# Kernel optimization log

Measured on AMD Instinct MI355X. Metric: run time of the kernel, lower is better.

The kernel has to match this reference:

```python
import jax, jax.numpy as jnp
import numpy as np

STRIDE = 1
PADDING = 1
KERNEL = 3


def _extract_patches(x, k, stride, padding):
    # x: [N, C, H, W] -> patches stacked as [k, k, N, C, Hout, Wout]
    xp = jnp.pad(x, ((0, 0), (0, 0), (padding, padding), (padding, padding)))
    Hp, Wp = xp.shape[2], xp.shape[3]
    oh = (Hp - k) // stride + 1
    ow = (Wp - k) // stride + 1
    rows = []
    for i in range(k):
        cols = []
        for j in range(k):
            cols.append(xp[:, :, i : i + oh * stride : stride, j : j + ow * stride : stride])
        rows.append(jnp.stack(cols, axis=0))
    return jnp.stack(rows, axis=0)  # [k, k, N, C, oh, ow]


def setup_inputs() -> dict:
    key = jax.random.key(0)
    k1, k2 = jax.random.split(key)
    N, C, H, W = 32, 32, 56, 56
    O, OH, OW, K = 32, 56, 56, 3
    x = jax.random.normal(k1, (N, C, H, W), dtype=jnp.float32)
    # kaiming-normal-ish scale for leaky_relu(a=0.1), fan_out mode
    fan_out = O * K * K
    gain = np.sqrt(2.0 / (1.0 + 0.1 ** 2))
    std = gain / np.sqrt(fan_out)
    weight = jax.random.normal(k2, (O, OH, OW, C, K, K), dtype=jnp.float32) * std
    bias = jnp.zeros((1, O, OH, OW), dtype=jnp.float32)
    return {"x": x, "weight": weight, "bias": bias}


def reference(x, weight, bias):
    # weight: [O, H, W, C, i, k]; patches: [i, k, N, C, H, W]
    patches = _extract_patches(x, KERNEL, STRIDE, PADDING)
    out = jnp.einsum('ohwcik,iknchw->nohw', weight, patches)
    return out + bias
```

## Files before the change

kernel.cpp:

```cpp
#include <hip/hip_runtime.h>

#define N_  32
#define C_  32
#define H_  56
#define W_  56
#define O_  32
#define HP_ 58
#define WP_ 58
#define HW_ (H_*W_)
#define CHW_ (C_*H_*W_)
#define KK_ 9
#define CKK_ (C_*KK_)

#define XT_FLOATS ((size_t)C_*HP_*WP_*N_)

typedef __bf16 bf16x8 __attribute__((ext_vector_type(8)));
typedef float  f32x4  __attribute__((ext_vector_type(4)));

__global__ __launch_bounds__(256) void xpose_kernel(const float* __restrict__ x,
                                                    float* __restrict__ xT) {
    const int c = blockIdx.x;
    const int y = blockIdx.y;
    __shared__ float sbuf[32 * 57];
    const int tid = threadIdx.x;
    const bool interior = (y >= 1) && (y <= H_);
    if (interior) {
        for (int idx = tid; idx < N_ * W_; idx += 256) {
            int n = idx / W_;
            int col = idx - n * W_;
            sbuf[n * 57 + col] = x[((size_t)(n * C_ + c) * H_ + (y - 1)) * W_ + col];
        }
    }
    __syncthreads();
    float* dst = xT + ((size_t)(c * HP_ + y)) * WP_ * N_;
    for (int idx = tid; idx < WP_ * N_; idx += 256) {
        int xx = idx >> 5;
        int n  = idx & 31;
        float v = 0.f;
        if (interior && xx >= 1 && xx <= W_) v = sbuf[n * 57 + (xx - 1)];
        dst[idx] = v;
    }
}

__global__ __launch_bounds__(256) void lc2d_mfma(const float* __restrict__ wgt,
                                                 const float* __restrict__ xT,
                                                 const float* __restrict__ bias,
                                                 float* __restrict__ out) {
    __shared__ int offs[288];
    __shared__ __align__(16) float sbuf[32][33][4];

    const int tid = threadIdx.x;
    for (int k = tid; k < 288; k += 256) {
        int c = k / 9, ij = k - 9 * c;
        int i = ij / 3, j = ij - 3 * i;
        offs[k] = c * (HP_ * WP_ * N_) + i * (WP_ * N_) + j * N_;
    }
    __syncthreads();

    const int flat = blockIdx.x;
    const int wg = (flat & 7) * 98 + (flat >> 3);
    const int wt = wg % 14;
    const int h  = wg / 14;
    const int wave = tid >> 6;
    const int lane = tid & 63;
    const int w = wt * 4 + wave;
    const int q = lane >> 4;
    const int r = lane & 15;

    const float* wb0 = wgt + ((size_t)(r * HW_ + h * W_ + w)) * CKK_ + 8 * q;
    const float* wb1 = wb0 + (size_t)16 * HW_ * CKK_;
    const float* ab = xT + (h * WP_ + w) * N_ + r;

    f32x4 acc00 = {0.f,0.f,0.f,0.f}, acc01 = {0.f,0.f,0.f,0.f};
    f32x4 acc10 = {0.f,0.f,0.f,0.f}, acc11 = {0.f,0.f,0.f,0.f};

    #pragma unroll 3
    for (int s = 0; s < 9; ++s) {
        const int4 ov0 = *(const int4*)&offs[32 * s + 8 * q];
        const int4 ov1 = *(const int4*)&offs[32 * s + 8 * q + 4];
        const float4 b0a = *(const float4*)(wb0 + 32 * s);
        const float4 b0b = *(const float4*)(wb0 + 32 * s + 4);
        const float4 b1a = *(const float4*)(wb1 + 32 * s);
        const float4 b1b = *(const float4*)(wb1 + 32 * s + 4);

        const int offv[8] = {ov0.x, ov0.y, ov0.z, ov0.w, ov1.x, ov1.y, ov1.z, ov1.w};
        float a0[8], a1[8];
        #pragma unroll
        for (int t = 0; t < 8; ++t) {
            const float* p = ab + offv[t];
            a0[t] = p[0];
            a1[t] = p[16];
        }

        bf16x8 af0, af1, bf0, bf1;
        #pragma unroll
        for (int t = 0; t < 8; ++t) {
            af0[t] = (__bf16)a0[t];
            af1[t] = (__bf16)a1[t];
        }
        bf0[0] = (__bf16)b0a.x; bf0[1] = (__bf16)b0a.y; bf0[2] = (__bf16)b0a.z; bf0[3] = (__bf16)b0a.w;
        bf0[4] = (__bf16)b0b.x; bf0[5] = (__bf16)b0b.y; bf0[6] = (__bf16)b0b.z; bf0[7] = (__bf16)b0b.w;
        bf1[0] = (__bf16)b1a.x; bf1[1] = (__bf16)b1a.y; bf1[2] = (__bf16)b1a.z; bf1[3] = (__bf16)b1a.w;
        bf1[4] = (__bf16)b1b.x; bf1[5] = (__bf16)b1b.y; bf1[6] = (__bf16)b1b.z; bf1[7] = (__bf16)b1b.w;

        acc00 = __builtin_amdgcn_mfma_f32_16x16x32_bf16(af0, bf0, acc00, 0, 0, 0);
        acc01 = __builtin_amdgcn_mfma_f32_16x16x32_bf16(af0, bf1, acc01, 0, 0, 0);
        acc10 = __builtin_amdgcn_mfma_f32_16x16x32_bf16(af1, bf0, acc10, 0, 0, 0);
        acc11 = __builtin_amdgcn_mfma_f32_16x16x32_bf16(af1, bf1, acc11, 0, 0, 0);
    }

    #pragma unroll
    for (int mt = 0; mt < 2; ++mt) {
        #pragma unroll
        for (int ot = 0; ot < 2; ++ot) {
            f32x4 a = (mt == 0) ? (ot == 0 ? acc00 : acc01)
                                : (ot == 0 ? acc10 : acc11);
            const int o = ot * 16 + r;
            #pragma unroll
            for (int reg = 0; reg < 4; ++reg) {
                const int n = mt * 16 + q * 4 + reg;
                sbuf[n][o][wave] = a[reg];
            }
        }
    }
    __syncthreads();

    const int w0 = wt * 4;
    #pragma unroll
    for (int rr = 0; rr < 4; ++rr) {
        const int fl = rr * 256 + tid;
        const int n = fl >> 5;
        const int o = fl & 31;
        float4 v = *(const float4*)&sbuf[n][o][0];
        const float4 bv = *(const float4*)(bias + o * HW_ + h * W_ + w0);
        v.x += bv.x; v.y += bv.y; v.z += bv.z; v.w += bv.w;
        *(float4*)(out + (size_t)n * CHW_ + o * HW_ + h * W_ + w0) = v;
    }
}

__global__ __launch_bounds__(256) void lc2d_naive(const float* __restrict__ x,
                                                  const float* __restrict__ wgt,
                                                  const float* __restrict__ bias,
                                                  float* __restrict__ out) {
    int idx = blockIdx.x * 256 + threadIdx.x;
    const int total = N_ * O_ * H_ * W_;
    if (idx >= total) return;
    int w = idx % W_;
    int h = (idx / W_) % H_;
    int o = (idx / HW_) % O_;
    int n = idx / CHW_;
    const float* wp = wgt + ((size_t)((o * H_ + h) * W_ + w)) * CKK_;
    float s = 0.f;
    for (int c = 0; c < C_; ++c) {
        for (int i = 0; i < 3; ++i) {
            int yy = h + i - 1;
            if (yy < 0 || yy >= H_) continue;
            for (int j = 0; j < 3; ++j) {
                int xx = w + j - 1;
                if (xx < 0 || xx >= W_) continue;
                s = fmaf(wp[c * KK_ + i * 3 + j],
                         x[((size_t)(n * C_ + c) * H_ + yy) * W_ + xx], s);
            }
        }
    }
    out[idx] = s + bias[idx % CHW_];
}

extern "C" void kernel_launch(void* const* d_in, const int* in_sizes, int n_in,
                              void* d_out, int out_size, void* d_ws, size_t ws_size,
                              hipStream_t stream) {
    const float* x    = (const float*)d_in[0];
    const float* wgt  = (const float*)d_in[1];
    const float* bias = (const float*)d_in[2];
    float* out = (float*)d_out;

    const size_t need = XT_FLOATS * sizeof(float);
    if (ws_size >= need) {
        float* xT = (float*)d_ws;
        hipLaunchKernelGGL(xpose_kernel, dim3(C_, HP_), dim3(256), 0, stream, x, xT);
        hipLaunchKernelGGL(lc2d_mfma, dim3(784), dim3(256), 0, stream, wgt, xT, bias, out);
    } else {
        int total = N_ * O_ * H_ * W_;
        hipLaunchKernelGGL(lc2d_naive, dim3((total + 255) / 256), dim3(256), 0, stream,
                           x, wgt, bias, out);
    }
}
```

Measured before the change: 45.37 us.

## Store transposed input as bf16 and split output channels across waves

The transpose kernel now writes the padded input workspace in bf16 rather than fp32. This halves its write and gather traffic and removes the per-element conversions in the main kernel. The MFMA kernel is also repartitioned: each block covers 2 output columns instead of 4, and each wave handles one 16-channel half of the outputs with 2 MFMAs instead of 4. The grid doubles to 1568 blocks and the epilogue uses float2 stores. The weight stream is unchanged, and the narrower output stores may coalesce less well.

```diff
diff --git a/kernel.cpp b/kernel.cpp
--- a/kernel.cpp
+++ b/kernel.cpp
@@ -12,13 +12,13 @@
 #define KK_ 9
 #define CKK_ (C_*KK_)
 
-#define XT_FLOATS ((size_t)C_*HP_*WP_*N_)
+#define XT_ELEMS ((size_t)C_*HP_*WP_*N_)
 
 typedef __bf16 bf16x8 __attribute__((ext_vector_type(8)));
 typedef float  f32x4  __attribute__((ext_vector_type(4)));
 
 __global__ __launch_bounds__(256) void xpose_kernel(const float* __restrict__ x,
-                                                    float* __restrict__ xT) {
+                                                    __bf16* __restrict__ xT) {
     const int c = blockIdx.x;
     const int y = blockIdx.y;
     __shared__ float sbuf[32 * 57];
@@ -32,22 +32,22 @@
         }
     }
     __syncthreads();
-    float* dst = xT + ((size_t)(c * HP_ + y)) * WP_ * N_;
+    __bf16* dst = xT + ((size_t)(c * HP_ + y)) * WP_ * N_;
     for (int idx = tid; idx < WP_ * N_; idx += 256) {
         int xx = idx >> 5;
         int n  = idx & 31;
         float v = 0.f;
         if (interior && xx >= 1 && xx <= W_) v = sbuf[n * 57 + (xx - 1)];
-        dst[idx] = v;
+        dst[idx] = (__bf16)v;
     }
 }
 
 __global__ __launch_bounds__(256) void lc2d_mfma(const float* __restrict__ wgt,
-                                                 const float* __restrict__ xT,
+                                                 const __bf16* __restrict__ xT,
                                                  const float* __restrict__ bias,
                                                  float* __restrict__ out) {
     __shared__ int offs[288];
-    __shared__ __align__(16) float sbuf[32][33][4];
+    __shared__ __align__(16) float sbuf[32][33][2];
 
     const int tid = threadIdx.x;
     for (int k = tid; k < 288; k += 256) {
@@ -58,83 +58,67 @@
     __syncthreads();
 
     const int flat = blockIdx.x;
-    const int wg = (flat & 7) * 98 + (flat >> 3);
-    const int wt = wg % 14;
-    const int h  = wg / 14;
+    const int wg = (flat & 7) * 196 + (flat >> 3);
+    const int wt = wg % 28;
+    const int h  = wg / 28;
     const int wave = tid >> 6;
     const int lane = tid & 63;
-    const int w = wt * 4 + wave;
+    const int dw = wave & 1;
+    const int oh = wave >> 1;
+    const int w  = wt * 2 + dw;
     const int q = lane >> 4;
     const int r = lane & 15;
 
-    const float* wb0 = wgt + ((size_t)(r * HW_ + h * W_ + w)) * CKK_ + 8 * q;
-    const float* wb1 = wb0 + (size_t)16 * HW_ * CKK_;
-    const float* ab = xT + (h * WP_ + w) * N_ + r;
+    const float* wb = wgt + ((size_t)((oh * 16 + r) * HW_ + h * W_ + w)) * CKK_ + 8 * q;
+    const __bf16* ab = xT + (h * WP_ + w) * N_ + r;
 
-    f32x4 acc00 = {0.f,0.f,0.f,0.f}, acc01 = {0.f,0.f,0.f,0.f};
-    f32x4 acc10 = {0.f,0.f,0.f,0.f}, acc11 = {0.f,0.f,0.f,0.f};
+    f32x4 acc0 = {0.f, 0.f, 0.f, 0.f};
+    f32x4 acc1 = {0.f, 0.f, 0.f, 0.f};
 
     #pragma unroll 3
     for (int s = 0; s < 9; ++s) {
         const int4 ov0 = *(const int4*)&offs[32 * s + 8 * q];
         const int4 ov1 = *(const int4*)&offs[32 * s + 8 * q + 4];
-        const float4 b0a = *(const float4*)(wb0 + 32 * s);
-        const float4 b0b = *(const float4*)(wb0 + 32 * s + 4);
-        const float4 b1a = *(const float4*)(wb1 + 32 * s);
-        const float4 b1b = *(const float4*)(wb1 + 32 * s + 4);
+        const float4 ba = *(const float4*)(wb + 32 * s);
+        const float4 bb = *(const float4*)(wb + 32 * s + 4);
 
         const int offv[8] = {ov0.x, ov0.y, ov0.z, ov0.w, ov1.x, ov1.y, ov1.z, ov1.w};
-        float a0[8], a1[8];
+        bf16x8 af0, af1, bfB;
         #pragma unroll
         for (int t = 0; t < 8; ++t) {
-            const float* p = ab + offv[t];
-            a0[t] = p[0];
-            a1[t] = p[16];
+            const __bf16* p = ab + offv[t];
+            af0[t] = p[0];
+            af1[t] = p[16];
         }
+        bfB[0] = (__bf16)ba.x; bfB[1] = (__bf16)ba.y; bfB[2] = (__bf16)ba.z; bfB[3] = (__bf16)ba.w;
+        bfB[4] = (__bf16)bb.x; bfB[5] = (__bf16)bb.y; bfB[6] = (__bf16)bb.z; bfB[7] = (__bf16)bb.w;
 
-        bf16x8 af0, af1, bf0, bf1;
-        #pragma unroll
-        for (int t = 0; t < 8; ++t) {
-            af0[t] = (__bf16)a0[t];
-            af1[t] = (__bf16)a1[t];
-        }
-        bf0[0] = (__bf16)b0a.x; bf0[1] = (__bf16)b0a.y; bf0[2] = (__bf16)b0a.z; bf0[3] = (__bf16)b0a.w;
-        bf0[4] = (__bf16)b0b.x; bf0[5] = (__bf16)b0b.y; bf0[6] = (__bf16)b0b.z; bf0[7] = (__bf16)b0b.w;
-        bf1[0] = (__bf16)b1a.x; bf1[1] = (__bf16)b1a.y; bf1[2] = (__bf16)b1a.z; bf1[3] = (__bf16)b1a.w;
-        bf1[4] = (__bf16)b1b.x; bf1[5] = (__bf16)b1b.y; bf1[6] = (__bf16)b1b.z; bf1[7] = (__bf16)b1b.w;
-
-        acc00 = __builtin_amdgcn_mfma_f32_16x16x32_bf16(af0, bf0, acc00, 0, 0, 0);
-        acc01 = __builtin_amdgcn_mfma_f32_16x16x32_bf16(af0, bf1, acc01, 0, 0, 0);
-        acc10 = __builtin_amdgcn_mfma_f32_16x16x32_bf16(af1, bf0, acc10, 0, 0, 0);
-        acc11 = __builtin_amdgcn_mfma_f32_16x16x32_bf16(af1, bf1, acc11, 0, 0, 0);
+        acc0 = __builtin_amdgcn_mfma_f32_16x16x32_bf16(af0, bfB, acc0, 0, 0, 0);
+        acc1 = __builtin_amdgcn_mfma_f32_16x16x32_bf16(af1, bfB, acc1, 0, 0, 0);
     }
 
     #pragma unroll
     for (int mt = 0; mt < 2; ++mt) {
+        f32x4 a = mt == 0 ? acc0 : acc1;
+        const int o = oh * 16 + r;
         #pragma unroll
-        for (int ot = 0; ot < 2; ++ot) {
-            f32x4 a = (mt == 0) ? (ot == 0 ? acc00 : acc01)
-                                : (ot == 0 ? acc10 : acc11);
-            const int o = ot * 16 + r;
-            #pragma unroll
-            for (int reg = 0; reg < 4; ++reg) {
-                const int n = mt * 16 + q * 4 + reg;
-                sbuf[n][o][wave] = a[reg];
-            }
+        for (int reg = 0; reg < 4; ++reg) {
+            const int n = mt * 16 + q * 4 + reg;
+            sbuf[n][o][dw] = a[reg];
         }
     }
     __syncthreads();
 
-    const int w0 = wt * 4;
+    const int w0 = wt * 2;
     #pragma unroll
     for (int rr = 0; rr < 4; ++rr) {
         const int fl = rr * 256 + tid;
         const int n = fl >> 5;
         const int o = fl & 31;
-        float4 v = *(const float4*)&sbuf[n][o][0];
-        const float4 bv = *(const float4*)(bias + o * HW_ + h * W_ + w0);
-        v.x += bv.x; v.y += bv.y; v.z += bv.z; v.w += bv.w;
-        *(float4*)(out + (size_t)n * CHW_ + o * HW_ + h * W_ + w0) = v;
+        float2 v = *(const float2*)&sbuf[n][o][0];
+        const float2 bv = *(const float2*)(bias + o * HW_ + h * W_ + w0);
+        v.x += bv.x; v.y += bv.y;
+        *(float2*)(out + (size_t)n * CHW_ + o * HW_ + h * W_ + w0) = v;
     }
 }
 
@@ -174,11 +158,11 @@
     const float* bias = (const float*)d_in[2];
     float* out = (float*)d_out;
 
-    const size_t need = XT_FLOATS * sizeof(float);
+    const size_t need = XT_ELEMS * sizeof(__bf16);
     if (ws_size >= need) {
-        float* xT = (float*)d_ws;
+        __bf16* xT = (__bf16*)d_ws;
         hipLaunchKernelGGL(xpose_kernel, dim3(C_, HP_), dim3(256), 0, stream, x, xT);
-        hipLaunchKernelGGL(lc2d_mfma, dim3(784), dim3(256), 0, stream, wgt, xT, bias, out);
+        hipLaunchKernelGGL(lc2d_mfma, dim3(1568), dim3(256), 0, stream, wgt, xT, bias, out);
     } else {
         int total = N_ * O_ * H_ * W_;
         hipLaunchKernelGGL(lc2d_naive, dim3((total + 255) / 256), dim3(256), 0, stream,
```

After: 42.67 us. 1.06x faster.
